# Kernel tuning notes

Hardware: AMD Instinct MI355X
Metric: run time of the kernel (lower is better)

## Reference

```python
import jax, jax.numpy as jnp
import numpy as np

NEG = -1e30  # safe stand-in for -inf in fp32


def _seg_logsumexp(scores, seg, num_segments):
    m = jax.ops.segment_max(scores, seg, num_segments=num_segments)
    m = jnp.maximum(m, NEG)
    s = jax.ops.segment_sum(jnp.exp(scores - m[seg]), seg, num_segments=num_segments)
    return jnp.where(s > 0, m + jnp.log(s), NEG)


def _chain_ll(x, length, src, dst, pdf, logw, init_lp, final_lp):
    # Log-domain HMM forward recursion over an edge-list graph.
    # x: [T, D] log-likelihoods; returns scalar log total path weight.
    S = init_lp.shape[0]
    T = x.shape[0]

    def step(alpha, inputs):
        xt, t = inputs
        scores = alpha[src] + logw + xt[pdf]          # [E]
        new_alpha = _seg_logsumexp(scores, dst, S)    # [S]
        alpha = jnp.where(t < length, new_alpha, alpha)
        return alpha, None

    alpha, _ = jax.lax.scan(step, init_lp, (x, jnp.arange(T)))
    return jax.nn.logsumexp(alpha + final_lp)


def chain_loss(x, x_lengths, den_src, den_dst, den_pdf, den_logw, den_init, den_final,
               num_src, num_dst, num_pdf, num_logw, num_init, num_final):
    # Denominator: one shared graph for all batch elements.
    den_ll = jax.vmap(_chain_ll, in_axes=(0, 0, None, None, None, None, None, None))(
        x, x_lengths, den_src, den_dst, den_pdf, den_logw, den_init, den_final)
    # Numerator: one graph per utterance.
    num_ll = jax.vmap(_chain_ll)(
        x, x_lengths, num_src, num_dst, num_pdf, num_logw, num_init, num_final)
    den_objf = jnp.sum(den_ll)
    num_objf = jnp.sum(num_ll)
    objf = -(num_objf - den_objf)
    return objf / jnp.sum(x_lengths).astype(x.dtype)  # avg=True


def setup_inputs() -> dict:
    key = jax.random.key(0)
    ks = jax.random.split(key, 16)
    B, T, D = 32, 500, 3072
    S_den, E_den = 4000, 120000
    S_num, E_num = 200, 600

    x = jax.random.normal(ks[0], (B, T, D), dtype=jnp.float32)
    x_lengths = jnp.sort(jax.random.randint(ks[1], (B,), T // 2, T + 1, dtype=jnp.int32))[::-1]

    den_src = jax.random.randint(ks[2], (E_den,), 0, S_den, dtype=jnp.int32)
    den_dst = jax.random.randint(ks[3], (E_den,), 0, S_den, dtype=jnp.int32)
    den_pdf = jax.random.randint(ks[4], (E_den,), 0, D, dtype=jnp.int32)
    den_logw = -5.0 * jax.random.uniform(ks[5], (E_den,), dtype=jnp.float32)
    den_init = -3.0 * jax.random.uniform(ks[6], (S_den,), dtype=jnp.float32)
    den_final = -3.0 * jax.random.uniform(ks[7], (S_den,), dtype=jnp.float32)

    num_src = jax.random.randint(ks[8], (B, E_num), 0, S_num, dtype=jnp.int32)
    num_dst = jax.random.randint(ks[9], (B, E_num), 0, S_num, dtype=jnp.int32)
    num_pdf = jax.random.randint(ks[10], (B, E_num), 0, D, dtype=jnp.int32)
    num_logw = -5.0 * jax.random.uniform(ks[11], (B, E_num), dtype=jnp.float32)
    num_init = -3.0 * jax.random.uniform(ks[12], (B, S_num), dtype=jnp.float32)
    num_final = -3.0 * jax.random.uniform(ks[13], (B, S_num), dtype=jnp.float32)

    return {"x": x, "x_lengths": x_lengths,
            "den_src": den_src, "den_dst": den_dst, "den_pdf": den_pdf,
            "den_logw": den_logw, "den_init": den_init, "den_final": den_final,
            "num_src": num_src, "num_dst": num_dst, "num_pdf": num_pdf,
            "num_logw": num_logw, "num_init": num_init, "num_final": num_final}


def reference(x, x_lengths, den_src, den_dst, den_pdf, den_logw, den_init, den_final,
              num_src, num_dst, num_pdf, num_logw, num_init, num_final):
    return chain_loss(x, x_lengths, den_src, den_dst, den_pdf, den_logw, den_init, den_final,
                      num_src, num_dst, num_pdf, num_logw, num_init, num_final)
```

## Files before the change

### kernel.cpp

```cpp
#include <hip/hip_runtime.h>

constexpr int B_     = 32;
constexpr int T_     = 500;
constexpr int D_     = 3072;
constexpr int S_DEN  = 4000;
constexpr int E_DEN  = 120000;
constexpr int S_NUM  = 200;
constexpr int E_NUM  = 600;
constexpr int NCHUNK = 8;
constexpr int WTGT   = (E_DEN + 2 * E_NUM) / NCHUNK;
constexpr int ECAP   = 15488;
constexpr int NTB    = 512;
constexpr int FLAGS_PER_UTT = 16;

__global__ void zero_ints(int* p, int n) {
    int i = blockIdx.x * 256 + threadIdx.x;
    if (i < n) p[i] = 0;
}

__global__ void hist_den(const int* __restrict__ dst, int* __restrict__ cnt) {
    int e = blockIdx.x * 256 + threadIdx.x;
    if (e < E_DEN) atomicAdd(&cnt[dst[e]], 1);
}

__global__ void hist_num(const int* __restrict__ dst, int* __restrict__ cnt) {
    int b = blockIdx.y, j = blockIdx.x * 256 + threadIdx.x;
    if (j < E_NUM) atomicAdd(&cnt[b * S_NUM + dst[b * E_NUM + j]], 1);
}

__global__ void scan_den(int* __restrict__ cnt_cur, int* __restrict__ row) {
    __shared__ int part[1024];
    int tid = threadIdx.x, base = tid * 4;
    int c[4], pre[4], s = 0;
    #pragma unroll
    for (int j = 0; j < 4; ++j) {
        int idx = base + j;
        c[j] = (idx < S_DEN) ? cnt_cur[idx] : 0;
        pre[j] = s; s += c[j];
    }
    part[tid] = s; __syncthreads();
    for (int off = 1; off < 1024; off <<= 1) {
        int v = (tid >= off) ? part[tid - off] : 0; __syncthreads();
        part[tid] += v; __syncthreads();
    }
    int offs = (tid > 0) ? part[tid - 1] : 0;
    #pragma unroll
    for (int j = 0; j < 4; ++j) {
        int idx = base + j;
        if (idx < S_DEN) { row[idx] = offs + pre[j]; cnt_cur[idx] = offs + pre[j]; }
    }
    if (tid == 1023) row[S_DEN] = part[1023];
}

__global__ void scan_num(int* __restrict__ cnt_cur, int* __restrict__ row) {
    __shared__ int part[256];
    int b = blockIdx.x, tid = threadIdx.x;
    int c = (tid < S_NUM) ? cnt_cur[b * S_NUM + tid] : 0;
    part[tid] = c; __syncthreads();
    for (int off = 1; off < 256; off <<= 1) {
        int v = (tid >= off) ? part[tid - off] : 0; __syncthreads();
        part[tid] += v; __syncthreads();
    }
    int excl = part[tid] - c;
    if (tid < S_NUM) { row[b * (S_NUM + 1) + tid] = excl; cnt_cur[b * S_NUM + tid] = excl; }
    if (tid == 255) row[b * (S_NUM + 1) + S_NUM] = part[255];
}

__global__ void scatter_den(const int* __restrict__ src, const int* __restrict__ dst,
                            const int* __restrict__ pdf, const float* __restrict__ logw,
                            int* __restrict__ cur, int2* __restrict__ csr) {
    int e = blockIdx.x * 256 + threadIdx.x;
    if (e >= E_DEN) return;
    int pos = atomicAdd(&cur[dst[e]], 1);
    csr[pos] = make_int2(src[e] | (pdf[e] << 12), __float_as_int(__expf(logw[e])));
}

__global__ void scatter_num(const int* __restrict__ src, const int* __restrict__ dst,
                            const int* __restrict__ pdf, const float* __restrict__ logw,
                            int* __restrict__ cur, int2* __restrict__ csr) {
    int b = blockIdx.y, j = blockIdx.x * 256 + threadIdx.x;
    if (j >= E_NUM) return;
    int e = b * E_NUM + j;
    int pos = atomicAdd(&cur[b * S_NUM + dst[e]], 1);
    csr[b * E_NUM + pos] = make_int2(src[e] | (pdf[e] << 12), __float_as_int(__expf(logw[e])));
}

__global__ void part_den(const int* __restrict__ row, int* __restrict__ part) {
    int r = threadIdx.x;
    if (r > NCHUNK) return;
    if (r == 0)        { part[0] = 0; return; }
    if (r == NCHUNK)   { part[NCHUNK] = S_DEN; return; }
    int target = r * WTGT; if (target > E_DEN) target = E_DEN;
    int lo = 0, hi = S_DEN;
    while (lo < hi) { int mid = (lo + hi) >> 1; if (row[mid] < target) lo = mid + 1; else hi = mid; }
    part[r] = lo;
}

__global__ __launch_bounds__(NTB, 1)
void chain_persist(const float* __restrict__ x, const int* __restrict__ x_lengths,
                   const int* __restrict__ den_row, const int2* __restrict__ den_csr,
                   const int* __restrict__ part,
                   const int* __restrict__ num_row, const int2* __restrict__ num_csr,
                   const float* __restrict__ den_init, const float* __restrict__ den_final,
                   const float* __restrict__ num_init, const float* __restrict__ num_final,
                   float* __restrict__ EAd,
                   unsigned long long* __restrict__ Mflag,
                   unsigned long long* __restrict__ Fflag,
                   float* __restrict__ ll) {
    __shared__ int2   csr_d[ECAP];
    __shared__ float4 ex4[D_ / 4];
    __shared__ float  eal[S_DEN];
    __shared__ int2   csr_n[E_NUM];
    __shared__ float  eal_n[S_NUM];
    __shared__ float  red[8], red_n[8];
    __shared__ float  s_m;
    float* ex = (float*)ex4;

    const int tid = threadIdx.x;
    const int b   = blockIdx.x & 31;
    const int r   = blockIdx.x >> 5;
    const int len = x_lengths[b];

    const int s0 = part[r], s1 = part[r + 1];
    const int e0 = den_row[s0], e1 = den_row[s1];
    const int ne = e1 - e0;
    for (int i = tid; i < ne; i += NTB) csr_d[i] = den_csr[e0 + i];
    const int sa = s0 + tid, sb = s0 + tid + NTB;
    int ba = 0, eaA = 0, bb = 0, ebB = 0;
    if (sa < s1) { ba = den_row[sa] - e0; eaA = den_row[sa + 1] - e0; }
    if (sb < s1) { bb = den_row[sb] - e0; ebB = den_row[sb + 1] - e0; }
    for (int s = tid; s < S_DEN; s += NTB) eal[s] = __expf(den_init[s]);

    int nb = 0, neE = 0;
    if (r == NCHUNK - 1) {
        for (int i = tid; i < E_NUM; i += NTB) csr_n[i] = num_csr[b * E_NUM + i];
        if (tid < S_NUM) {
            nb  = num_row[b * (S_NUM + 1) + tid];
            neE = num_row[b * (S_NUM + 1) + tid + 1];
            eal_n[tid] = __expf(num_init[b * S_NUM + tid]);
        }
    }

    const float* xb = x + (size_t)b * T_ * D_;
    const bool  has2 = tid < (D_ / 4 - NTB);
    float4 xr0, xr1;
    {
        const float4* p = (const float4*)xb;
        xr0 = p[tid];
        xr1 = has2 ? p[tid + NTB] : make_float4(0.f, 0.f, 0.f, 0.f);
        float4 ev;
        ev.x = __expf(fminf(xr0.x, 60.f)); ev.y = __expf(fminf(xr0.y, 60.f));
        ev.z = __expf(fminf(xr0.z, 60.f)); ev.w = __expf(fminf(xr0.w, 60.f));
        ex4[tid] = ev;
        if (has2) {
            float4 e1v;
            e1v.x = __expf(fminf(xr1.x, 60.f)); e1v.y = __expf(fminf(xr1.y, 60.f));
            e1v.z = __expf(fminf(xr1.z, 60.f)); e1v.w = __expf(fminf(xr1.w, 60.f));
            ex4[tid + NTB] = e1v;
        }
        if (len > 1) {
            const float4* pn = (const float4*)(xb + (size_t)D_);
            xr0 = pn[tid];
            if (has2) xr1 = pn[tid + NTB];
        }
    }
    __syncthreads();

    float off = 0.f, offn = 0.f, acc0 = 0.f, acc1 = 0.f, accn = 0.f;
    unsigned long long* uflag = Mflag + (size_t)b * FLAGS_PER_UTT;

    for (int t = 0; t < len; ++t) {
        float lmax = 0.f;
        acc0 = 0.f; acc1 = 0.f;
        if (sa < s1) {
            float a0 = 0.f, a1 = 0.f;
            int e = ba;
            for (; e + 2 <= eaA; e += 2) {
                int2 p0 = csr_d[e], p1 = csr_d[e + 1];
                a0 += eal[p0.x & 0xFFF] * __int_as_float(p0.y) * ex[p0.x >> 12];
                a1 += eal[p1.x & 0xFFF] * __int_as_float(p1.y) * ex[p1.x >> 12];
            }
            if (e < eaA) {
                int2 p0 = csr_d[e];
                a0 += eal[p0.x & 0xFFF] * __int_as_float(p0.y) * ex[p0.x >> 12];
            }
            acc0 = a0 + a1; lmax = acc0;
        }
        if (sb < s1) {
            float a0 = 0.f, a1 = 0.f;
            int e = bb;
            for (; e + 2 <= ebB; e += 2) {
                int2 p0 = csr_d[e], p1 = csr_d[e + 1];
                a0 += eal[p0.x & 0xFFF] * __int_as_float(p0.y) * ex[p0.x >> 12];
                a1 += eal[p1.x & 0xFFF] * __int_as_float(p1.y) * ex[p1.x >> 12];
            }
            if (e < ebB) {
                int2 p0 = csr_d[e];
                a0 += eal[p0.x & 0xFFF] * __int_as_float(p0.y) * ex[p0.x >> 12];
            }
            acc1 = a0 + a1; lmax = fmaxf(lmax, acc1);
        }

        float* EAn_g = EAd + ((size_t)((t + 1) & 1) * B_ + b) * S_DEN;
        if (sa < s1) __hip_atomic_store(&EAn_g[sa], acc0, __ATOMIC_RELAXED, __HIP_MEMORY_SCOPE_AGENT);
        if (sb < s1) __hip_atomic_store(&EAn_g[sb], acc1, __ATOMIC_RELAXED, __HIP_MEMORY_SCOPE_AGENT);

        float lmax_n = 0.f;
        if (r == NCHUNK - 1 && tid < S_NUM) {
            float a = 0.f;
            for (int e = nb; e < neE; ++e) {
                int2 p0 = csr_n[e];
                a += eal_n[p0.x & 0xFFF] * __int_as_float(p0.y) * ex[p0.x >> 12];
            }
            accn = a; lmax_n = a;
        }

        #pragma unroll
        for (int o = 32; o > 0; o >>= 1) {
            lmax   = fmaxf(lmax,   __shfl_down(lmax, o));
            lmax_n = fmaxf(lmax_n, __shfl_down(lmax_n, o));
        }
        if ((tid & 63) == 0) { red[tid >> 6] = lmax; red_n[tid >> 6] = lmax_n; }
        __syncthreads();

        if (t + 1 < len && tid == 0) {
            float bm = red[0];
            #pragma unroll
            for (int w = 1; w < 8; ++w) bm = fmaxf(bm, red[w]);
            unsigned long long pv =
                ((unsigned long long)(unsigned)(t + 1) << 32) |
                (unsigned long long)__float_as_uint(bm);
            __hip_atomic_store(&uflag[(t & 1) * 8 + r], pv,
                               __ATOMIC_RELEASE, __HIP_MEMORY_SCOPE_AGENT);
        }

        if (r == NCHUNK - 1) {
            float Mn = red_n[0];
            #pragma unroll
            for (int w = 1; w < 8; ++w) Mn = fmaxf(Mn, red_n[w]);
            if (!(Mn > 0.f)) Mn = 1.f;
            if (tid < S_NUM) eal_n[tid] = accn / Mn;
            offn += __logf(Mn);
        }
        if (t + 1 < len) {
            float4 ev;
            ev.x = __expf(fminf(xr0.x, 60.f)); ev.y = __expf(fminf(xr0.y, 60.f));
            ev.z = __expf(fminf(xr0.z, 60.f)); ev.w = __expf(fminf(xr0.w, 60.f));
            ex4[tid] = ev;
            if (has2) {
                float4 e1v;
                e1v.x = __expf(fminf(xr1.x, 60.f)); e1v.y = __expf(fminf(xr1.y, 60.f));
                e1v.z = __expf(fminf(xr1.z, 60.f)); e1v.w = __expf(fminf(xr1.w, 60.f));
                ex4[tid + NTB] = e1v;
            }
            if (t + 2 < len) {
                const float4* pn = (const float4*)(xb + (size_t)(t + 2) * D_);
                xr0 = pn[tid];
                if (has2) xr1 = pn[tid + NTB];
            }

            if (tid < 64) {
                unsigned long long* slots = &uflag[(t & 1) * 8];
                float mv = 0.f;
                bool rdy = (tid >= 8);
                const unsigned want = (unsigned)(t + 1);
                while (true) {
                    if (!rdy) {
                        unsigned long long v = __hip_atomic_load(&slots[tid],
                                                 __ATOMIC_RELAXED, __HIP_MEMORY_SCOPE_AGENT);
                        if ((unsigned)(v >> 32) == want) {
                            rdy = true; mv = __uint_as_float((unsigned)v);
                        }
                    }
                    if (__all(rdy)) break;
                    __builtin_amdgcn_s_sleep(1);
                }
                #pragma unroll
                for (int o = 4; o > 0; o >>= 1) mv = fmaxf(mv, __shfl_down(mv, o));
                if (tid == 0) s_m = (mv > 0.f) ? mv : 1.f;
            }
            __syncthreads();

            float M = s_m;
            off += __logf(M);
            float inv = 1.f / M;
            float v[8];
            #pragma unroll
            for (int k = 0; k < 8; ++k) {
                int s = tid + k * NTB;
                v[k] = (s < S_DEN)
                     ? __hip_atomic_load(&EAn_g[s], __ATOMIC_RELAXED, __HIP_MEMORY_SCOPE_AGENT)
                     : 0.f;
            }
            #pragma unroll
            for (int k = 0; k < 8; ++k) {
                int s = tid + k * NTB;
                if (s < S_DEN) eal[s] = v[k] * inv;
            }
            __syncthreads();
        }
    }

    float fs = 0.f;
    if (sa < s1) fs += acc0 * __expf(den_final[sa]);
    if (sb < s1) fs += acc1 * __expf(den_final[sb]);
    #pragma unroll
    for (int o = 32; o > 0; o >>= 1) fs += __shfl_down(fs, o);
    if ((tid & 63) == 0) red[tid >> 6] = fs;
    __syncthreads();

    if (tid == 0) {
        float bf = 0.f;
        #pragma unroll
        for (int w = 0; w < 8; ++w) bf += red[w];
        unsigned long long pv = ((unsigned long long)(unsigned)len << 32) |
                                (unsigned long long)__float_as_uint(bf);
        __hip_atomic_store(&Fflag[b * 8 + r], pv, __ATOMIC_RELEASE, __HIP_MEMORY_SCOPE_AGENT);
    }

    if (r == 0 && tid < 64) {
        float sv = 0.f;
        bool rdy = (tid >= 8);
        const unsigned want = (unsigned)len;
        while (true) {
            if (!rdy) {
                unsigned long long v = __hip_atomic_load(&Fflag[b * 8 + tid],
                                         __ATOMIC_RELAXED, __HIP_MEMORY_SCOPE_AGENT);
                if ((unsigned)(v >> 32) == want) { rdy = true; sv = __uint_as_float((unsigned)v); }
            }
            if (__all(rdy)) break;
            __builtin_amdgcn_s_sleep(1);
        }
        #pragma unroll
        for (int o = 4; o > 0; o >>= 1) sv += __shfl_down(sv, o);
        if (tid == 0) ll[b] = __logf(sv) + off;
    }

    if (r == NCHUNK - 1) {
        float ns = (tid < S_NUM) ? eal_n[tid] * __expf(num_final[b * S_NUM + tid]) : 0.f;
        #pragma unroll
        for (int o = 32; o > 0; o >>= 1) ns += __shfl_down(ns, o);
        if ((tid & 63) == 0) red_n[tid >> 6] = ns;
        __syncthreads();
        if (tid == 0) {
            float tn = 0.f;
            #pragma unroll
            for (int w = 0; w < 8; ++w) tn += red_n[w];
            ll[B_ + b] = __logf(tn) + offn;
        }
    }
}

__global__ void finalize_loss(const float* __restrict__ ll, const int* __restrict__ x_lengths,
                              float* __restrict__ out) {
    int tid = threadIdx.x;
    float d = (tid < B_) ? ll[tid] : 0.f;
    float n = (tid < B_) ? ll[B_ + tid] : 0.f;
    float l = (tid < B_) ? (float)x_lengths[tid] : 0.f;
    #pragma unroll
    for (int o = 32; o > 0; o >>= 1) {
        d += __shfl_down(d, o); n += __shfl_down(n, o); l += __shfl_down(l, o);
    }
    if (tid == 0) out[0] = (d - n) / l;
}

__global__ __launch_bounds__(1024)
void chain_forward_atomic(const float* __restrict__ x, const int* __restrict__ x_lengths,
                          const int* __restrict__ den_src, const int* __restrict__ den_dst,
                          const int* __restrict__ den_pdf, const float* __restrict__ den_logw,
                          const float* __restrict__ den_init, const float* __restrict__ den_final,
                          const int* __restrict__ num_src, const int* __restrict__ num_dst,
                          const int* __restrict__ num_pdf, const float* __restrict__ num_logw,
                          const float* __restrict__ num_init, const float* __restrict__ num_final,
                          float* __restrict__ ll_out) {
    __shared__ float ea[S_DEN];
    __shared__ float ssum[S_DEN];
    __shared__ float ex[D_];
    __shared__ float red[16];
    __shared__ float s_m;
    const int  tid = threadIdx.x;
    const bool is_den = blockIdx.x < B_;
    const int  b = is_den ? blockIdx.x : blockIdx.x - B_;
    const int  S = is_den ? S_DEN : S_NUM;
    const int  E = is_den ? E_DEN : E_NUM;
    const int*   esrc = is_den ? den_src : num_src + b * E_NUM;
    const int*   edst = is_den ? den_dst : num_dst + b * E_NUM;
    const int*   epdf = is_den ? den_pdf : num_pdf + b * E_NUM;
    const float* elw  = is_den ? den_logw: num_logw + b * E_NUM;
    const float* init = is_den ? den_init : num_init + b * S_NUM;
    const float* fin  = is_den ? den_final: num_final + b * S_NUM;
    const int    len  = x_lengths[b];
    const float* xb   = x + (size_t)b * T_ * D_;
    for (int s = tid; s < S; s += 1024) { ea[s] = __expf(init[s]); ssum[s] = 0.f; }
    float off = 0.f;
    for (int t = 0; t < len; ++t) {
        const float4* xr4 = reinterpret_cast<const float4*>(xb + (size_t)t * D_);
        for (int d = tid; d < D_ / 4; d += 1024) {
            float4 v = xr4[d];
            ex[4*d+0] = __expf(fminf(v.x, 60.f)); ex[4*d+1] = __expf(fminf(v.y, 60.f));
            ex[4*d+2] = __expf(fminf(v.z, 60.f)); ex[4*d+3] = __expf(fminf(v.w, 60.f));
        }
        __syncthreads();
        for (int e = tid; e < E; e += 1024)
            unsafeAtomicAdd(&ssum[edst[e]], ea[esrc[e]] * __expf(elw[e]) * ex[epdf[e]]);
        __syncthreads();
        float lm = 0.f;
        for (int s = tid; s < S; s += 1024) lm = fmaxf(lm, ssum[s]);
        #pragma unroll
        for (int o = 32; o > 0; o >>= 1) lm = fmaxf(lm, __shfl_down(lm, o));
        if ((tid & 63) == 0) red[tid >> 6] = lm;
        __syncthreads();
        if (tid == 0) {
            float m = red[0];
            for (int w = 1; w < 16; ++w) m = fmaxf(m, red[w]);
            s_m = (m > 0.f) ? m : 1.f;
        }
        __syncthreads();
        float inv = 1.f / s_m;
        off += __logf(s_m);
        for (int s = tid; s < S; s += 1024) { ea[s] = ssum[s] * inv; ssum[s] = 0.f; }
    }
    float lsum = 0.f;
    for (int s = tid; s < S; s += 1024) lsum += ea[s] * __expf(fin[s]);
    #pragma unroll
    for (int o = 32; o > 0; o >>= 1) lsum += __shfl_down(lsum, o);
    if ((tid & 63) == 0) red[tid >> 6] = lsum;
    __syncthreads();
    if (tid == 0) {
        float tot = 0.f;
        for (int w = 0; w < 16; ++w) tot += red[w];
        ll_out[blockIdx.x] = off + __logf(tot);
    }
}

static inline size_t align16(size_t v) { return (v + 15) & ~size_t(15); }

extern "C" void kernel_launch(void* const* d_in, const int* in_sizes, int n_in,
                              void* d_out, int out_size, void* d_ws, size_t ws_size,
                              hipStream_t stream) {
    const float* x         = (const float*)d_in[0];
    const int*   x_lengths = (const int*)  d_in[1];
    const int*   den_src   = (const int*)  d_in[2];
    const int*   den_dst   = (const int*)  d_in[3];
    const int*   den_pdf   = (const int*)  d_in[4];
    const float* den_logw  = (const float*)d_in[5];
    const float* den_init  = (const float*)d_in[6];
    const float* den_final = (const float*)d_in[7];
    const int*   num_src   = (const int*)  d_in[8];
    const int*   num_dst   = (const int*)  d_in[9];
    const int*   num_pdf   = (const int*)  d_in[10];
    const float* num_logw  = (const float*)d_in[11];
    const float* num_init  = (const float*)d_in[12];
    const float* num_final = (const float*)d_in[13];

    char* ws = (char*)d_ws;
    size_t o = 0;
    float*              ll      = (float*)             (ws + o); o = align16(o + 64 * sizeof(float));
    int*                den_row = (int*)               (ws + o); o = align16(o + (S_DEN + 1) * sizeof(int));
    int*                den_cur = (int*)               (ws + o); o = align16(o + S_DEN * sizeof(int));
    int*                num_row = (int*)               (ws + o); o = align16(o + B_ * (S_NUM + 1) * sizeof(int));
    int*                num_cur = (int*)               (ws + o); o = align16(o + B_ * S_NUM * sizeof(int));
    int2*               den_csr = (int2*)              (ws + o); o = align16(o + (size_t)E_DEN * sizeof(int2));
    int2*               num_csr = (int2*)              (ws + o); o = align16(o + (size_t)B_ * E_NUM * sizeof(int2));
    int*                part    = (int*)               (ws + o); o = align16(o + (NCHUNK + 1) * sizeof(int));
    float*              EAd     = (float*)             (ws + o); o = align16(o + (size_t)2 * B_ * S_DEN * sizeof(float));
    unsigned long long* Mflag   = (unsigned long long*)(ws + o); o = align16(o + (size_t)B_ * FLAGS_PER_UTT * sizeof(unsigned long long));
    unsigned long long* Fflag   = (unsigned long long*)(ws + o); o = align16(o + (size_t)B_ * 8 * sizeof(unsigned long long));
    const size_t need = o;

    if (ws_size >= need) {
        zero_ints<<<(S_DEN + 255) / 256, 256, 0, stream>>>(den_cur, S_DEN);
        zero_ints<<<(B_ * S_NUM + 255) / 256, 256, 0, stream>>>(num_cur, B_ * S_NUM);
        hist_den<<<(E_DEN + 255) / 256, 256, 0, stream>>>(den_dst, den_cur);
        hist_num<<<dim3(3, B_), 256, 0, stream>>>(num_dst, num_cur);
        scan_den<<<1, 1024, 0, stream>>>(den_cur, den_row);
        scan_num<<<B_, 256, 0, stream>>>(num_cur, num_row);
        scatter_den<<<(E_DEN + 255) / 256, 256, 0, stream>>>(
            den_src, den_dst, den_pdf, den_logw, den_cur, den_csr);
        scatter_num<<<dim3(3, B_), 256, 0, stream>>>(
            num_src, num_dst, num_pdf, num_logw, num_cur, num_csr);
        part_den<<<1, 16, 0, stream>>>(den_row, part);

        void* args[] = {
            (void*)&x, (void*)&x_lengths, (void*)&den_row, (void*)&den_csr, (void*)&part,
            (void*)&num_row, (void*)&num_csr, (void*)&den_init, (void*)&den_final,
            (void*)&num_init, (void*)&num_final, (void*)&EAd, (void*)&Mflag,
            (void*)&Fflag, (void*)&ll
        };
        hipError_t err = hipLaunchCooperativeKernel((const void*)chain_persist,
                                                    dim3(B_ * NCHUNK), dim3(NTB),
                                                    args, 0, stream);
        if (err != hipSuccess) {
            chain_persist<<<dim3(B_ * NCHUNK), dim3(NTB), 0, stream>>>(
                x, x_lengths, den_row, den_csr, part, num_row, num_csr,
                den_init, den_final, num_init, num_final,
                EAd, Mflag, Fflag, ll);
        }
        finalize_loss<<<1, 64, 0, stream>>>(ll, x_lengths, (float*)d_out);
    } else {
        chain_forward_atomic<<<2 * B_, 1024, 0, stream>>>(
            x, x_lengths, den_src, den_dst, den_pdf, den_logw, den_init, den_final,
            num_src, num_dst, num_pdf, num_logw, num_init, num_final, ll);
        finalize_loss<<<1, 64, 0, stream>>>(ll, x_lengths, (float*)d_out);
    }
}
```

Baseline: 3.671 ms.

## Replace per-step max flags with tagged alpha slots and deferred normalization

Each chunk block now writes its alpha values as 64-bit words that carry the timestep tag, and every block polls those tagged slots directly. This removes the separate release-flag exchange of per-chunk maxima and the second pass that reloaded alpha. The max over the gathered alpha is computed locally after the gather, and the division by it is applied at the next step through inv_prev. This drops one block-wide barrier and one cross-block round trip per timestep, at the cost of doubling the exchanged data size and spinning on all 4000 slots per block.

```diff
diff --git a/kernel.cpp b/kernel.cpp
--- a/kernel.cpp
+++ b/kernel.cpp
@@ -11,7 +11,6 @@
 constexpr int WTGT   = (E_DEN + 2 * E_NUM) / NCHUNK;
 constexpr int ECAP   = 15488;
 constexpr int NTB    = 512;
-constexpr int FLAGS_PER_UTT = 16;
 
 __global__ void zero_ints(int* p, int n) {
     int i = blockIdx.x * 256 + threadIdx.x;
@@ -103,8 +102,7 @@
                    const int* __restrict__ num_row, const int2* __restrict__ num_csr,
                    const float* __restrict__ den_init, const float* __restrict__ den_final,
                    const float* __restrict__ num_init, const float* __restrict__ num_final,
-                   float* __restrict__ EAd,
-                   unsigned long long* __restrict__ Mflag,
+                   unsigned long long* __restrict__ EAslot,
                    unsigned long long* __restrict__ Fflag,
                    float* __restrict__ ll) {
     __shared__ int2   csr_d[ECAP];
@@ -113,7 +111,6 @@
     __shared__ int2   csr_n[E_NUM];
     __shared__ float  eal_n[S_NUM];
     __shared__ float  red[8], red_n[8];
-    __shared__ float  s_m;
     float* ex = (float*)ex4;
 
     const int tid = threadIdx.x;
@@ -167,11 +164,10 @@
     __syncthreads();
 
     float off = 0.f, offn = 0.f, acc0 = 0.f, acc1 = 0.f, accn = 0.f;
-    unsigned long long* uflag = Mflag + (size_t)b * FLAGS_PER_UTT;
+    float inv_prev = 1.f;
 
     for (int t = 0; t < len; ++t) {
-        float lmax = 0.f;
-        acc0 = 0.f; acc1 = 0.f;
+        float raw0 = 0.f, raw1 = 0.f;
         if (sa < s1) {
             float a0 = 0.f, a1 = 0.f;
             int e = ba;
@@ -184,7 +180,7 @@
                 int2 p0 = csr_d[e];
                 a0 += eal[p0.x & 0xFFF] * __int_as_float(p0.y) * ex[p0.x >> 12];
             }
-            acc0 = a0 + a1; lmax = acc0;
+            raw0 = a0 + a1;
         }
         if (sb < s1) {
             float a0 = 0.f, a1 = 0.f;
@@ -198,41 +194,37 @@
                 int2 p0 = csr_d[e];
                 a0 += eal[p0.x & 0xFFF] * __int_as_float(p0.y) * ex[p0.x >> 12];
             }
-            acc1 = a0 + a1; lmax = fmaxf(lmax, acc1);
-        }
-
-        float* EAn_g = EAd + ((size_t)((t + 1) & 1) * B_ + b) * S_DEN;
-        if (sa < s1) __hip_atomic_store(&EAn_g[sa], acc0, __ATOMIC_RELAXED, __HIP_MEMORY_SCOPE_AGENT);
-        if (sb < s1) __hip_atomic_store(&EAn_g[sb], acc1, __ATOMIC_RELAXED, __HIP_MEMORY_SCOPE_AGENT);
+            raw1 = a0 + a1;
+        }
+        acc0 = raw0 * inv_prev;
+        acc1 = raw1 * inv_prev;
+
+        if (t + 1 < len) {
+            unsigned long long* slw = EAslot + ((size_t)(t & 1) * B_ + b) * S_DEN;
+            const unsigned long long tg = (unsigned long long)(unsigned)(t + 1) << 32;
+            if (sa < s1)
+                __hip_atomic_store(&slw[sa], tg | __float_as_uint(acc0),
+                                   __ATOMIC_RELAXED, __HIP_MEMORY_SCOPE_AGENT);
+            if (sb < s1)
+                __hip_atomic_store(&slw[sb], tg | __float_as_uint(acc1),
+                                   __ATOMIC_RELAXED, __HIP_MEMORY_SCOPE_AGENT);
+        }
 
         float lmax_n = 0.f;
-        if (r == NCHUNK - 1 && tid < S_NUM) {
-            float a = 0.f;
-            for (int e = nb; e < neE; ++e) {
-                int2 p0 = csr_n[e];
-                a += eal_n[p0.x & 0xFFF] * __int_as_float(p0.y) * ex[p0.x >> 12];
-            }
-            accn = a; lmax_n = a;
-        }
-
-        #pragma unroll
-        for (int o = 32; o > 0; o >>= 1) {
-            lmax   = fmaxf(lmax,   __shfl_down(lmax, o));
-            lmax_n = fmaxf(lmax_n, __shfl_down(lmax_n, o));
-        }
-        if ((tid & 63) == 0) { red[tid >> 6] = lmax; red_n[tid >> 6] = lmax_n; }
-        __syncthreads();
-
-        if (t + 1 < len && tid == 0) {
-            float bm = red[0];
+        if (r == NCHUNK - 1) {
+            if (tid < S_NUM) {
+                float a = 0.f;
+                for (int e = nb; e < neE; ++e) {
+                    int2 p0 = csr_n[e];
+                    a += eal_n[p0.x & 0xFFF] * __int_as_float(p0.y) * ex[p0.x >> 12];
+                }
+                accn = a; lmax_n = a;
+            }
             #pragma unroll
-            for (int w = 1; w < 8; ++w) bm = fmaxf(bm, red[w]);
-            unsigned long long pv =
-                ((unsigned long long)(unsigned)(t + 1) << 32) |
-                (unsigned long long)__float_as_uint(bm);
-            __hip_atomic_store(&uflag[(t & 1) * 8 + r], pv,
-                               __ATOMIC_RELEASE, __HIP_MEMORY_SCOPE_AGENT);
-        }
+            for (int o = 32; o > 0; o >>= 1) lmax_n = fmaxf(lmax_n, __shfl_down(lmax_n, o));
+            if ((tid & 63) == 0) red_n[tid >> 6] = lmax_n;
+        }
+        __syncthreads();
 
         if (r == NCHUNK - 1) {
             float Mn = red_n[0];
@@ -242,6 +234,7 @@
             if (tid < S_NUM) eal_n[tid] = accn / Mn;
             offn += __logf(Mn);
         }
+
         if (t + 1 < len) {
             float4 ev;
             ev.x = __expf(fminf(xr0.x, 60.f)); ev.y = __expf(fminf(xr0.y, 60.f));
@@ -259,45 +252,38 @@
                 if (has2) xr1 = pn[tid + NTB];
             }
 
-            if (tid < 64) {
-                unsigned long long* slots = &uflag[(t & 1) * 8];
-                float mv = 0.f;
-                bool rdy = (tid >= 8);
-                const unsigned want = (unsigned)(t + 1);
-                while (true) {
-                    if (!rdy) {
-                        unsigned long long v = __hip_atomic_load(&slots[tid],
-                                                 __ATOMIC_RELAXED, __HIP_MEMORY_SCOPE_AGENT);
-                        if ((unsigned)(v >> 32) == want) {
-                            rdy = true; mv = __uint_as_float((unsigned)v);
-                        }
+            const unsigned long long* slr = EAslot + ((size_t)(t & 1) * B_ + b) * S_DEN;
+            const unsigned want = (unsigned)(t + 1);
+            float mv = 0.f;
+            unsigned rdy = 0;
+            while (rdy != 0xFFu) {
+                #pragma unroll
+                for (int k = 0; k < 8; ++k) {
+                    if (rdy & (1u << k)) continue;
+                    int s = tid + k * NTB;
+                    if (s >= S_DEN) { rdy |= 1u << k; continue; }
+                    unsigned long long v = __hip_atomic_load(&slr[s],
+                                             __ATOMIC_RELAXED, __HIP_MEMORY_SCOPE_AGENT);
+                    if ((unsigned)(v >> 32) == want) {
+                        float f = __uint_as_float((unsigned)v);
+                        eal[s] = f;
+                        mv = fmaxf(mv, f);
+                        rdy |= 1u << k;
                     }
-                    if (__all(rdy)) break;
-                    __builtin_amdgcn_s_sleep(1);
                 }
-                #pragma unroll
-                for (int o = 4; o > 0; o >>= 1) mv = fmaxf(mv, __shfl_down(mv, o));
-                if (tid == 0) s_m = (mv > 0.f) ? mv : 1.f;
-            }
+                if (rdy != 0xFFu) __builtin_amdgcn_s_sleep(1);
+            }
+            #pragma unroll
+            for (int o = 32; o > 0; o >>= 1) mv = fmaxf(mv, __shfl_down(mv, o));
+            if ((tid & 63) == 0) red[tid >> 6] = mv;
             __syncthreads();
 
-            float M = s_m;
+            float M = red[0];
+            #pragma unroll
+            for (int w = 1; w < 8; ++w) M = fmaxf(M, red[w]);
+            if (!(M > 0.f)) M = 1.f;
             off += __logf(M);
-            float inv = 1.f / M;
-            float v[8];
-            #pragma unroll
-            for (int k = 0; k < 8; ++k) {
-                int s = tid + k * NTB;
-                v[k] = (s < S_DEN)
-                     ? __hip_atomic_load(&EAn_g[s], __ATOMIC_RELAXED, __HIP_MEMORY_SCOPE_AGENT)
-                     : 0.f;
-            }
-            #pragma unroll
-            for (int k = 0; k < 8; ++k) {
-                int s = tid + k * NTB;
-                if (s < S_DEN) eal[s] = v[k] * inv;
-            }
-            __syncthreads();
+            inv_prev = 1.f / M;
         }
     }
 
@@ -315,7 +301,7 @@
         for (int w = 0; w < 8; ++w) bf += red[w];
         unsigned long long pv = ((unsigned long long)(unsigned)len << 32) |
                                 (unsigned long long)__float_as_uint(bf);
-        __hip_atomic_store(&Fflag[b * 8 + r], pv, __ATOMIC_RELEASE, __HIP_MEMORY_SCOPE_AGENT);
+        __hip_atomic_store(&Fflag[b * 8 + r], pv, __ATOMIC_RELAXED, __HIP_MEMORY_SCOPE_AGENT);
     }
 
     if (r == 0 && tid < 64) {
@@ -463,8 +449,7 @@
     int2*               den_csr = (int2*)              (ws + o); o = align16(o + (size_t)E_DEN * sizeof(int2));
     int2*               num_csr = (int2*)              (ws + o); o = align16(o + (size_t)B_ * E_NUM * sizeof(int2));
     int*                part    = (int*)               (ws + o); o = align16(o + (NCHUNK + 1) * sizeof(int));
-    float*              EAd     = (float*)             (ws + o); o = align16(o + (size_t)2 * B_ * S_DEN * sizeof(float));
-    unsigned long long* Mflag   = (unsigned long long*)(ws + o); o = align16(o + (size_t)B_ * FLAGS_PER_UTT * sizeof(unsigned long long));
+    unsigned long long* EAslot  = (unsigned long long*)(ws + o); o = align16(o + (size_t)2 * B_ * S_DEN * sizeof(unsigned long long));
     unsigned long long* Fflag   = (unsigned long long*)(ws + o); o = align16(o + (size_t)B_ * 8 * sizeof(unsigned long long));
     const size_t need = o;
 
@@ -484,7 +469,7 @@
         void* args[] = {
             (void*)&x, (void*)&x_lengths, (void*)&den_row, (void*)&den_csr, (void*)&part,
             (void*)&num_row, (void*)&num_csr, (void*)&den_init, (void*)&den_final,
-            (void*)&num_init, (void*)&num_final, (void*)&EAd, (void*)&Mflag,
+            (void*)&num_init, (void*)&num_final, (void*)&EAslot,
             (void*)&Fflag, (void*)&ll
         };
         hipError_t err = hipLaunchCooperativeKernel((const void*)chain_persist,
@@ -494,7 +479,7 @@
             chain_persist<<<dim3(B_ * NCHUNK), dim3(NTB), 0, stream>>>(
                 x, x_lengths, den_row, den_csr, part, num_row, num_csr,
                 den_init, den_final, num_init, num_final,
-                EAd, Mflag, Fflag, ll);
+                EAslot, Fflag, ll);
         }
         finalize_loss<<<1, 64, 0, stream>>>(ll, x_lengths, (float*)d_out);
     } else {
```

New measurement: 3.385 ms, median of 2. -7.8%, faster.
